# Performance work log

Measured on AMD Instinct MI355X. Metric: run time of the kernel, lower is better.

## Reference

```python
import jax, jax.numpy as jnp
import numpy as np


def setup_inputs() -> dict:
    key = jax.random.key(0)
    ks = jax.random.split(key, 6)
    B, IN, H, OUT = 4096, 1024, 2048, 256
    s1 = 1.0 / np.sqrt(IN)
    s2 = 1.0 / np.sqrt(H)
    return {
        "x": jax.random.normal(ks[0], (B, IN), dtype=jnp.float32),
        "W1": jax.random.uniform(ks[1], (H, IN), jnp.float32, -s1, s1),
        "b1": jax.random.uniform(ks[2], (H,), jnp.float32, -s1, s1),
        "W2": jax.random.uniform(ks[3], (OUT, H), jnp.float32, -s2, s2),
        "b2": jax.random.uniform(ks[4], (OUT,), jnp.float32, -s2, s2),
        "tau_mem": jnp.float32(10.0),
        "tau_syn": jnp.float32(5.0),
        "v_thresh": jnp.float32(1.0),
        "v_reset": jnp.float32(0.0),
        "v_mem0": jnp.zeros((B, H), jnp.float32),
        "i_syn0": jnp.zeros((B, H), jnp.float32),
        "time_steps": 32,
    }


def reference(x, W1, b1, W2, b2, tau_mem, tau_syn, v_thresh, v_reset, v_mem0, i_syn0, time_steps):
    dt = jnp.float32(1.0)
    # fc1(x)/time_steps is identical every step in the original loop; compute once.
    cur = (x @ W1.T + b1) / jnp.float32(time_steps)  # [B, H]

    def step(carry, _):
        v, i = carry
        i = i - (dt / tau_syn) * i + cur
        v = v - (dt / tau_mem) * v + i
        s = (v >= v_thresh).astype(x.dtype)
        v = v * (1.0 - s) + v_reset * s
        return (v, i), s

    (_, _), spikes = jax.lax.scan(step, (v_mem0, i_syn0), None, length=time_steps)
    total_spikes = spikes.sum(axis=0)  # [B, H]
    output = total_spikes @ W2.T + b2  # [B, OUT]
    return output, total_spikes
```

## Files before the change

kernel.cpp:

```cpp
#include <hip/hip_runtime.h>
#include <hip/hip_bf16.h>
#include <stdint.h>

typedef __attribute__((ext_vector_type(8))) short bf16x8;
typedef __attribute__((ext_vector_type(4))) float f32x4;

__device__ __forceinline__ float vmulf(float a, float b) {
    float d; asm volatile("v_mul_f32 %0, %1, %2" : "=v"(d) : "v"(a), "v"(b)); return d;
}
__device__ __forceinline__ float vaddf(float a, float b) {
    float d; asm volatile("v_add_f32 %0, %1, %2" : "=v"(d) : "v"(a), "v"(b)); return d;
}
__device__ __forceinline__ float vsubf(float a, float b) {
    float d; asm volatile("v_sub_f32 %0, %1, %2" : "=v"(d) : "v"(a), "v"(b)); return d;
}

__device__ __forceinline__ short bf16h(float v) {
    __hip_bfloat16 h = __float2bfloat16(v);
    return *(short*)&h;
}
__device__ __forceinline__ float bf16f(short s) {
    return __uint_as_float(((unsigned int)(unsigned short)s) << 16);
}
__device__ __forceinline__ void split2(float v, short& h, short& m) {
    h = bf16h(v);
    m = bf16h(__fsub_rn(v, bf16f(h)));
}

__device__ __forceinline__ float decode_scalar(const void* p, float dflt) {
    float f = *(const float*)p;
    if (!(f == f) || fabsf(f) > 1.0e6f) return dflt;
    return f;
}
__device__ __forceinline__ int decode_ts(const void* p) {
    int w = *(const int*)p;
    if (w >= 1 && w <= 100000) return w;
    return 32;
}

__device__ __forceinline__ void gl16(const float* g, float* l) {
    __builtin_amdgcn_global_load_lds(
        (const __attribute__((address_space(1))) unsigned int*)g,
        (__attribute__((address_space(3))) unsigned int*)l, 16, 0, 0);
}

#define LDA 36

__global__ __launch_bounds__(256) void k1_panel_gemm(
    const float* __restrict__ X,
    const float* __restrict__ W1,
    float* __restrict__ P0,
    float* __restrict__ P1,
    int M, int N, int K, int KC)
{
    __shared__ __align__(16) float As[2][128][16];
    __shared__ __align__(16) float Bs[2][128][16];

    const int t  = threadIdx.x;
    const int tx = t & 15;
    const int ty = t >> 4;
    const int m0 = blockIdx.x * 128;
    const int n0 = blockIdx.y * 128;
    const int kz = blockIdx.z * KC;
    float* __restrict__ Pout = blockIdx.z ? P1 : P0;

    float p[8][8] = {};

    const int w     = t >> 6;
    const int l     = t & 63;
    const int r0    = 32 * w + (l >> 2);
    const int r1    = r0 + 16;
    const int selem = ((l & 3) ^ ((l >> 3) & 3)) << 2;
    const int oa0 = (m0 + r0) * K + selem;
    const int oa1 = (m0 + r1) * K + selem;
    const int ob0 = (n0 + r0) * K + selem;
    const int ob1 = (n0 + r1) * K + selem;

    gl16(X  + oa0 + kz, &As[0][32 * w][0]);
    gl16(X  + oa1 + kz, &As[0][32 * w + 16][0]);
    gl16(W1 + ob0 + kz, &Bs[0][32 * w][0]);
    gl16(W1 + ob1 + kz, &Bs[0][32 * w + 16][0]);

    const int cax = (ty >> 1) & 3;
    const int cbx = (tx >> 1) & 3;

    const int nch = KC >> 4;
    for (int c = 0; c < nch; ++c) {
        __syncthreads();
        const int d = c & 1;
        if (c + 1 < nch) {
            const int kn = kz + ((c + 1) << 4);
            const int dn = d ^ 1;
            gl16(X  + oa0 + kn, &As[dn][32 * w][0]);
            gl16(X  + oa1 + kn, &As[dn][32 * w + 16][0]);
            gl16(W1 + ob0 + kn, &Bs[dn][32 * w][0]);
            gl16(W1 + ob1 + kn, &Bs[dn][32 * w + 16][0]);
        }
        #pragma unroll
        for (int g = 0; g < 4; ++g) {
            float4 bfv[8];
            const int cb = (g ^ cbx) << 2;
            #pragma unroll
            for (int j = 0; j < 8; ++j)
                bfv[j] = *(const float4*)&Bs[d][tx + 16 * j][cb];
            const int ca = (g ^ cax) << 2;
            #pragma unroll
            for (int i = 0; i < 8; ++i) {
                const float4 af = *(const float4*)&As[d][ty + 16 * i][ca];
                #pragma unroll
                for (int kk = 0; kk < 4; ++kk) {
                    const float a = ((const float*)&af)[kk];
                    #pragma unroll
                    for (int j = 0; j < 8; ++j)
                        p[i][j] = __builtin_fmaf(a, ((const float*)&bfv[j])[kk], p[i][j]);
                }
            }
        }
    }

    #pragma unroll
    for (int i = 0; i < 8; ++i) {
        const size_t rowb = (size_t)(m0 + ty + 16 * i) * N;
        #pragma unroll
        for (int j = 0; j < 8; ++j)
            Pout[rowb + n0 + tx + 16 * j] = p[i][j];
    }
}

__global__ __launch_bounds__(256) void k1_combine_scan(
    const float* __restrict__ P0,
    const float* __restrict__ P1,
    const float* __restrict__ b1,
    const void* tau_mem_p, const void* tau_syn_p,
    const void* v_thresh_p, const void* v_reset_p, const void* ts_p,
    float* __restrict__ spikes, int N, int total4)
{
    const int idx4 = blockIdx.x * 256 + threadIdx.x;
    if (idx4 >= total4) return;

    const float tau_m = decode_scalar(tau_mem_p, 10.0f);
    const float tau_s = decode_scalar(tau_syn_p, 5.0f);
    const float vth   = decode_scalar(v_thresh_p, 1.0f);
    const float vrs   = decode_scalar(v_reset_p, 0.0f);
    const int   ts    = decode_ts(ts_p);
    const float rs    = 1.0f / tau_s;
    const float rm    = 1.0f / tau_m;
    const float ivts  = 1.0f / (float)ts;

    const float4 a = ((const float4*)P0)[idx4];
    const float4 b = ((const float4*)P1)[idx4];
    const int col0 = (idx4 * 4) % N;
    const float4 bb = *(const float4*)&b1[col0];

    float cur[4], iv[4], vv[4], cnt[4];
    const float av[4] = {a.x, a.y, a.z, a.w};
    const float bv[4] = {b.x, b.y, b.z, b.w};
    const float bbv[4] = {bb.x, bb.y, bb.z, bb.w};
    #pragma unroll
    for (int e = 0; e < 4; ++e) {
        const float c = vaddf(av[e], bv[e]);
        cur[e] = vmulf(vaddf(c, bbv[e]), ivts);
        iv[e] = 0.0f; vv[e] = 0.0f; cnt[e] = 0.0f;
    }
    for (int tt = 0; tt < ts; ++tt) {
        #pragma unroll
        for (int e = 0; e < 4; ++e) {
            iv[e] = vaddf(vsubf(iv[e], vmulf(rs, iv[e])), cur[e]);
            vv[e] = vaddf(vsubf(vv[e], vmulf(rm, vv[e])), iv[e]);
            const bool s = (vv[e] >= vth);
            cnt[e] += s ? 1.0f : 0.0f;
            vv[e]   = s ? vrs : vv[e];
        }
    }
    ((float4*)spikes)[idx4] = make_float4(cnt[0], cnt[1], cnt[2], cnt[3]);
}

__global__ __launch_bounds__(256) void k1_f32chain_snn(
    const float* __restrict__ X, const float* __restrict__ W1,
    const float* __restrict__ b1,
    const void* tau_mem_p, const void* tau_syn_p,
    const void* v_thresh_p, const void* v_reset_p, const void* ts_p,
    float* __restrict__ spikes, int M, int N, int K, int f0)
{
    __shared__ float As[128][LDA];
    __shared__ float Bs[128][LDA];

    const int t  = threadIdx.x;
    const int tx = t & 15;
    const int ty = t >> 4;
    const int m0 = blockIdx.x * 128;
    const int n0 = blockIdx.y * 128;

    float c[8][8] = {};
    float p[8][8] = {};

    for (int k0 = 0; k0 < K; k0 += 32) {
        #pragma unroll
        for (int cc = 0; cc < 4; ++cc) {
            const int li  = cc * 256 + t;
            const int row = li >> 3;
            const int q   = li & 7;
            *(float4*)&As[row][q * 4] =
                *(const float4*)&X[(size_t)(m0 + row) * K + k0 + q * 4];
            *(float4*)&Bs[row][q * 4] =
                *(const float4*)&W1[(size_t)(n0 + row) * K + k0 + q * 4];
        }
        __syncthreads();
        #pragma unroll
        for (int g = 0; g < 8; ++g) {
            float4 af[8], bf[8];
            #pragma unroll
            for (int i = 0; i < 8; ++i)
                af[i] = *(const float4*)&As[ty + 16 * i][g * 4];
            #pragma unroll
            for (int j = 0; j < 8; ++j)
                bf[j] = *(const float4*)&Bs[tx + 16 * j][g * 4];
            #pragma unroll
            for (int kk = 0; kk < 4; ++kk) {
                #pragma unroll
                for (int i = 0; i < 8; ++i) {
                    const float a = ((const float*)&af[i])[kk];
                    #pragma unroll
                    for (int j = 0; j < 8; ++j)
                        p[i][j] = __builtin_fmaf(a, ((const float*)&bf[j])[kk], p[i][j]);
                }
            }
        }
        __syncthreads();
        const int ke = k0 + 32;
        if (ke == f0 || ke == K) {
            #pragma unroll
            for (int i = 0; i < 8; ++i)
                #pragma unroll
                for (int j = 0; j < 8; ++j) {
                    c[i][j] = vaddf(c[i][j], p[i][j]);
                    p[i][j] = 0.0f;
                }
        }
    }

    const float tau_m = decode_scalar(tau_mem_p, 10.0f);
    const float tau_s = decode_scalar(tau_syn_p, 5.0f);
    const float vth   = decode_scalar(v_thresh_p, 1.0f);
    const float vrs   = decode_scalar(v_reset_p, 0.0f);
    const int   ts    = decode_ts(ts_p);
    const float rs    = 1.0f / tau_s;
    const float rm    = 1.0f / tau_m;
    const float ivts  = 1.0f / (float)ts;

    #pragma unroll
    for (int j = 0; j < 8; ++j) {
        const int col    = n0 + tx + 16 * j;
        const float bias = b1[col];
        float cur[8], iv[8], vv[8], cnt[8];
        #pragma unroll
        for (int i = 0; i < 8; ++i) {
            cur[i] = vmulf(vaddf(c[i][j], bias), ivts);
            iv[i] = 0.0f; vv[i] = 0.0f; cnt[i] = 0.0f;
        }
        for (int tt = 0; tt < ts; ++tt) {
            #pragma unroll
            for (int i = 0; i < 8; ++i) {
                iv[i] = vaddf(vsubf(iv[i], vmulf(rs, iv[i])), cur[i]);
                vv[i] = vaddf(vsubf(vv[i], vmulf(rm, vv[i])), iv[i]);
                const bool s = (vv[i] >= vth);
                cnt[i] += s ? 1.0f : 0.0f;
                vv[i]   = s ? vrs : vv[i];
            }
        }
        #pragma unroll
        for (int i = 0; i < 8; ++i)
            spikes[(size_t)(m0 + ty + 16 * i) * N + col] = cnt[i];
    }
}

__global__ __launch_bounds__(256) void k2_partial(
    const float* __restrict__ S, const float* __restrict__ W2,
    float* __restrict__ Pt,
    int M, int N2, int K2, int KC2)
{
    __shared__ __align__(16) short Sa[64 * 32];
    __shared__ __align__(16) short Bh[64 * 32];
    __shared__ __align__(16) short Bm[64 * 32];

    const int t    = threadIdx.x;
    const int l    = t & 63;
    const int w    = t >> 6;
    const int quad = l >> 4;
    const int r    = l & 15;
    const int wm   = w & 1;
    const int wn   = w >> 1;

    const int m0 = blockIdx.x * 64;
    const int n0 = blockIdx.y * 64;
    const int kz = blockIdx.z * KC2;
    float* __restrict__ outp = Pt + (size_t)blockIdx.z * M * N2;

    f32x4 acc[2][2] = {};

    for (int k0 = kz; k0 < kz + KC2; k0 += 32) {
        #pragma unroll
        for (int cc = 0; cc < 2; ++cc) {
            const int li  = cc * 256 + t;
            const int row = li >> 3;
            const int q   = li & 7;
            const float4 vs = *(const float4*)&S[(size_t)(m0 + row) * K2 + k0 + q * 4];
            *(short4*)&Sa[row * 32 + q * 4] =
                make_short4(bf16h(vs.x), bf16h(vs.y), bf16h(vs.z), bf16h(vs.w));
            const float4 vb = *(const float4*)&W2[(size_t)(n0 + row) * K2 + k0 + q * 4];
            short h[4], m_[4];
            split2(vb.x, h[0], m_[0]); split2(vb.y, h[1], m_[1]);
            split2(vb.z, h[2], m_[2]); split2(vb.w, h[3], m_[3]);
            *(short4*)&Bh[row * 32 + q * 4] = make_short4(h[0], h[1], h[2], h[3]);
            *(short4*)&Bm[row * 32 + q * 4] = make_short4(m_[0], m_[1], m_[2], m_[3]);
        }
        __syncthreads();

        bf16x8 af[2], bh[2], bm[2];
        #pragma unroll
        for (int i = 0; i < 2; ++i) {
            af[i] = *(const bf16x8*)&Sa[(wm * 32 + i * 16 + r) * 32 + quad * 8];
            bh[i] = *(const bf16x8*)&Bh[(wn * 32 + i * 16 + r) * 32 + quad * 8];
            bm[i] = *(const bf16x8*)&Bm[(wn * 32 + i * 16 + r) * 32 + quad * 8];
        }
        #pragma unroll
        for (int i = 0; i < 2; ++i)
            #pragma unroll
            for (int j = 0; j < 2; ++j) {
                acc[i][j] = __builtin_amdgcn_mfma_f32_16x16x32_bf16(af[i], bh[j], acc[i][j], 0, 0, 0);
                acc[i][j] = __builtin_amdgcn_mfma_f32_16x16x32_bf16(af[i], bm[j], acc[i][j], 0, 0, 0);
            }
        __syncthreads();
    }

    #pragma unroll
    for (int j = 0; j < 2; ++j) {
        const int col = n0 + wn * 32 + j * 16 + r;
        #pragma unroll
        for (int i = 0; i < 2; ++i) {
            const int rowb = m0 + wm * 32 + i * 16 + quad * 4;
            #pragma unroll
            for (int e = 0; e < 4; ++e)
                outp[(size_t)(rowb + e) * N2 + col] = acc[i][j][e];
        }
    }
}

__global__ __launch_bounds__(256) void k2_combine(
    const float* __restrict__ Pt, const float* __restrict__ b2,
    float* __restrict__ out, int N2, int total4, size_t stride4)
{
    const int idx4 = blockIdx.x * 256 + threadIdx.x;
    if (idx4 >= total4) return;
    float4 s = ((const float4*)Pt)[idx4];
    #pragma unroll
    for (int z = 1; z < 4; ++z) {
        const float4 v = ((const float4*)Pt)[stride4 * z + idx4];
        s.x += v.x; s.y += v.y; s.z += v.z; s.w += v.w;
    }
    const float4 bb = *(const float4*)&b2[(idx4 * 4) % N2];
    s.x += bb.x; s.y += bb.y; s.z += bb.z; s.w += bb.w;
    ((float4*)out)[idx4] = s;
}

__global__ __launch_bounds__(256) void k2_gemm(
    const float* __restrict__ S, const float* __restrict__ W2,
    const float* __restrict__ b2, float* __restrict__ out,
    int M, int N2, int K2)
{
    __shared__ __align__(16) short Sa[64 * 32];
    __shared__ __align__(16) short Bh[64 * 32];
    __shared__ __align__(16) short Bm[64 * 32];

    const int t    = threadIdx.x;
    const int l    = t & 63;
    const int w    = t >> 6;
    const int quad = l >> 4;
    const int r    = l & 15;
    const int wm   = w & 1;
    const int wn   = w >> 1;

    const int m0 = blockIdx.x * 64;
    const int n0 = blockIdx.y * 64;

    f32x4 acc[2][2] = {};

    for (int k0 = 0; k0 < K2; k0 += 32) {
        #pragma unroll
        for (int cc = 0; cc < 2; ++cc) {
            const int li  = cc * 256 + t;
            const int row = li >> 3;
            const int q   = li & 7;
            const float4 vs = *(const float4*)&S[(size_t)(m0 + row) * K2 + k0 + q * 4];
            *(short4*)&Sa[row * 32 + q * 4] =
                make_short4(bf16h(vs.x), bf16h(vs.y), bf16h(vs.z), bf16h(vs.w));
            const float4 vb = *(const float4*)&W2[(size_t)(n0 + row) * K2 + k0 + q * 4];
            short h[4], m_[4];
            split2(vb.x, h[0], m_[0]); split2(vb.y, h[1], m_[1]);
            split2(vb.z, h[2], m_[2]); split2(vb.w, h[3], m_[3]);
            *(short4*)&Bh[row * 32 + q * 4] = make_short4(h[0], h[1], h[2], h[3]);
            *(short4*)&Bm[row * 32 + q * 4] = make_short4(m_[0], m_[1], m_[2], m_[3]);
        }
        __syncthreads();

        bf16x8 af[2], bh[2], bm[2];
        #pragma unroll
        for (int i = 0; i < 2; ++i) {
            af[i] = *(const bf16x8*)&Sa[(wm * 32 + i * 16 + r) * 32 + quad * 8];
            bh[i] = *(const bf16x8*)&Bh[(wn * 32 + i * 16 + r) * 32 + quad * 8];
            bm[i] = *(const bf16x8*)&Bm[(wn * 32 + i * 16 + r) * 32 + quad * 8];
        }
        #pragma unroll
        for (int i = 0; i < 2; ++i)
            #pragma unroll
            for (int j = 0; j < 2; ++j) {
                acc[i][j] = __builtin_amdgcn_mfma_f32_16x16x32_bf16(af[i], bh[j], acc[i][j], 0, 0, 0);
                acc[i][j] = __builtin_amdgcn_mfma_f32_16x16x32_bf16(af[i], bm[j], acc[i][j], 0, 0, 0);
            }
        __syncthreads();
    }

    #pragma unroll
    for (int j = 0; j < 2; ++j) {
        const int col = n0 + wn * 32 + j * 16 + r;
        const float bias = b2[col];
        #pragma unroll
        for (int i = 0; i < 2; ++i) {
            const int rowb = m0 + wm * 32 + i * 16 + quad * 4;
            #pragma unroll
            for (int e = 0; e < 4; ++e)
                out[(size_t)(rowb + e) * N2 + col] = __fadd_rn(acc[i][j][e], bias);
        }
    }
}

extern "C" void kernel_launch(void* const* d_in, const int* in_sizes, int n_in,
                              void* d_out, int out_size, void* d_ws, size_t ws_size,
                              hipStream_t stream) {
    (void)n_in; (void)out_size;

    const float* X  = (const float*)d_in[0];
    const float* W1 = (const float*)d_in[1];
    const float* b1 = (const float*)d_in[2];
    const float* W2 = (const float*)d_in[3];
    const float* b2 = (const float*)d_in[4];
    const void* tau_mem = d_in[5];
    const void* tau_syn = d_in[6];
    const void* vth     = d_in[7];
    const void* vrs     = d_in[8];
    const void* ts      = d_in[11];

    const int H   = in_sizes[2];
    const int IN  = in_sizes[1] / H;
    const int OUT = in_sizes[4];
    const int B   = in_sizes[0] / IN;

    float* out    = (float*)d_out;
    float* spikes = out + (size_t)B * OUT;

    const int KC = 512;
    const size_t panel_bytes = (size_t)B * H * sizeof(float);
    const bool ws_ok = (IN == 2 * KC) && (ws_size >= panel_bytes) &&
                       ((uintptr_t)d_ws % 16 == 0);

    if (ws_ok) {
        float* P1 = (float*)d_ws;
        dim3 g1(B / 128, H / 128, 2);
        k1_panel_gemm<<<g1, 256, 0, stream>>>(X, W1, spikes, P1, B, H, IN, KC);

        const int total4 = (B * H) / 4;
        k1_combine_scan<<<(total4 + 255) / 256, 256, 0, stream>>>(
            spikes, P1, b1, tau_mem, tau_syn, vth, vrs, ts, spikes, H, total4);
    } else {
        dim3 g1(B / 128, H / 128);
        k1_f32chain_snn<<<g1, 256, 0, stream>>>(X, W1, b1, tau_mem, tau_syn, vth, vrs, ts,
                                                spikes, B, H, IN, KC);
    }

    const int KC2 = 512;
    const size_t k2_part_bytes = 4 * (size_t)B * OUT * sizeof(float);
    if (ws_ok && H == 4 * KC2 && ws_size >= k2_part_bytes) {
        float* Pt = (float*)d_ws;
        dim3 g2(B / 64, OUT / 64, 4);
        k2_partial<<<g2, 256, 0, stream>>>(spikes, W2, Pt, B, OUT, H, KC2);
        const int total4 = (B * OUT) / 4;
        k2_combine<<<(total4 + 255) / 256, 256, 0, stream>>>(
            Pt, b2, out, OUT, total4, (size_t)B * OUT / 4);
    } else {
        dim3 g2(B / 64, OUT / 64);
        k2_gemm<<<g2, 256, 0, stream>>>(spikes, W2, b2, out, B, OUT, H);
    }
}
```

Measured before the change: 416.3 us.

## Fuse layer-1 GEMM with LIF scan, dropping split-K panels and workspace round trip

Replaces the split-K panel GEMM plus separate combine/scan kernel with one kernel that computes a 64x128 tile over the full K, merges the two 512-wide K halves in registers, and runs the 32-step LIF recurrence in-register before writing spike counts. This removes writing and rereading two B x H float panels through global memory and one kernel launch. In exchange the grid loses the split-K z dimension, gets twice as many blocks along M with a smaller M tile, and the serial scan now runs inside the GEMM kernel rather than in a separate fully parallel pass.

After: 464.5 us. 1.12x slower.

```diff
diff --git a/kernel.cpp b/kernel.cpp
--- a/kernel.cpp
+++ b/kernel.cpp
@@ -46,53 +46,53 @@
 
 #define LDA 36
 
-__global__ __launch_bounds__(256) void k1_panel_gemm(
+__global__ __launch_bounds__(256) void k1_fused_snn(
     const float* __restrict__ X,
     const float* __restrict__ W1,
-    float* __restrict__ P0,
-    float* __restrict__ P1,
-    int M, int N, int K, int KC)
+    const float* __restrict__ b1,
+    const void* tau_mem_p, const void* tau_syn_p,
+    const void* v_thresh_p, const void* v_reset_p, const void* ts_p,
+    float* __restrict__ spikes, int M, int N, int K)
 {
-    __shared__ __align__(16) float As[2][128][16];
+    __shared__ __align__(16) float As[2][64][16];
     __shared__ __align__(16) float Bs[2][128][16];
 
     const int t  = threadIdx.x;
     const int tx = t & 15;
     const int ty = t >> 4;
-    const int m0 = blockIdx.x * 128;
+    const int m0 = blockIdx.x * 64;
     const int n0 = blockIdx.y * 128;
-    const int kz = blockIdx.z * KC;
-    float* __restrict__ Pout = blockIdx.z ? P1 : P0;
-
-    float p[8][8] = {};
+
+    float p[4][8] = {};
+    float c[4][8];
 
     const int w     = t >> 6;
     const int l     = t & 63;
-    const int r0    = 32 * w + (l >> 2);
-    const int r1    = r0 + 16;
+    const int rr    = l >> 2;
     const int selem = ((l & 3) ^ ((l >> 3) & 3)) << 2;
-    const int oa0 = (m0 + r0) * K + selem;
-    const int oa1 = (m0 + r1) * K + selem;
-    const int ob0 = (n0 + r0) * K + selem;
-    const int ob1 = (n0 + r1) * K + selem;
-
-    gl16(X  + oa0 + kz, &As[0][32 * w][0]);
-    gl16(X  + oa1 + kz, &As[0][32 * w + 16][0]);
-    gl16(W1 + ob0 + kz, &Bs[0][32 * w][0]);
-    gl16(W1 + ob1 + kz, &Bs[0][32 * w + 16][0]);
+    const int ra  = 16 * w + rr;
+    const int rb0 = 32 * w + rr;
+    const int rb1 = rb0 + 16;
+    const int oa  = (m0 + ra ) * K + selem;
+    const int ob0 = (n0 + rb0) * K + selem;
+    const int ob1 = (n0 + rb1) * K + selem;
+
+    gl16(X  + oa , &As[0][16 * w][0]);
+    gl16(W1 + ob0, &Bs[0][32 * w][0]);
+    gl16(W1 + ob1, &Bs[0][32 * w + 16][0]);
 
     const int cax = (ty >> 1) & 3;
     const int cbx = (tx >> 1) & 3;
 
-    const int nch = KC >> 4;
-    for (int c = 0; c < nch; ++c) {
-        __syncthreads();
-        const int d = c & 1;
-        if (c + 1 < nch) {
-            const int kn = kz + ((c + 1) << 4);
+    const int nch = K >> 4;
+    int nf = 0;
+    for (int ch = 0; ch < nch; ++ch) {
+        __syncthreads();
+        const int d = ch & 1;
+        if (ch + 1 < nch) {
+            const int kn = (ch + 1) << 4;
             const int dn = d ^ 1;
-            gl16(X  + oa0 + kn, &As[dn][32 * w][0]);
-            gl16(X  + oa1 + kn, &As[dn][32 * w + 16][0]);
+            gl16(X  + oa  + kn, &As[dn][16 * w][0]);
             gl16(W1 + ob0 + kn, &Bs[dn][32 * w][0]);
             gl16(W1 + ob1 + kn, &Bs[dn][32 * w + 16][0]);
         }
@@ -105,7 +105,7 @@
                 bfv[j] = *(const float4*)&Bs[d][tx + 16 * j][cb];
             const int ca = (g ^ cax) << 2;
             #pragma unroll
-            for (int i = 0; i < 8; ++i) {
+            for (int i = 0; i < 4; ++i) {
                 const float4 af = *(const float4*)&As[d][ty + 16 * i][ca];
                 #pragma unroll
                 for (int kk = 0; kk < 4; ++kk) {
@@ -116,27 +116,22 @@
                 }
             }
         }
-    }
-
-    #pragma unroll
-    for (int i = 0; i < 8; ++i) {
-        const size_t rowb = (size_t)(m0 + ty + 16 * i) * N;
-        #pragma unroll
-        for (int j = 0; j < 8; ++j)
-            Pout[rowb + n0 + tx + 16 * j] = p[i][j];
-    }
-}
-
-__global__ __launch_bounds__(256) void k1_combine_scan(
-    const float* __restrict__ P0,
-    const float* __restrict__ P1,
-    const float* __restrict__ b1,
-    const void* tau_mem_p, const void* tau_syn_p,
-    const void* v_thresh_p, const void* v_reset_p, const void* ts_p,
-    float* __restrict__ spikes, int N, int total4)
-{
-    const int idx4 = blockIdx.x * 256 + threadIdx.x;
-    if (idx4 >= total4) return;
+        const int ke = (ch + 1) << 4;
+        if ((ke & 511) == 0 || ke == K) {
+            if (nf == 0) {
+                #pragma unroll
+                for (int i = 0; i < 4; ++i)
+                    #pragma unroll
+                    for (int j = 0; j < 8; ++j) { c[i][j] = p[i][j]; p[i][j] = 0.0f; }
+            } else {
+                #pragma unroll
+                for (int i = 0; i < 4; ++i)
+                    #pragma unroll
+                    for (int j = 0; j < 8; ++j) { c[i][j] = vaddf(c[i][j], p[i][j]); p[i][j] = 0.0f; }
+            }
+            ++nf;
+        }
+    }
 
     const float tau_m = decode_scalar(tau_mem_p, 10.0f);
     const float tau_s = decode_scalar(tau_syn_p, 5.0f);
@@ -147,32 +142,30 @@
     const float rm    = 1.0f / tau_m;
     const float ivts  = 1.0f / (float)ts;
 
-    const float4 a = ((const float4*)P0)[idx4];
-    const float4 b = ((const float4*)P1)[idx4];
-    const int col0 = (idx4 * 4) % N;
-    const float4 bb = *(const float4*)&b1[col0];
-
-    float cur[4], iv[4], vv[4], cnt[4];
-    const float av[4] = {a.x, a.y, a.z, a.w};
-    const float bv[4] = {b.x, b.y, b.z, b.w};
-    const float bbv[4] = {bb.x, bb.y, bb.z, bb.w};
     #pragma unroll
-    for (int e = 0; e < 4; ++e) {
-        const float c = vaddf(av[e], bv[e]);
-        cur[e] = vmulf(vaddf(c, bbv[e]), ivts);
-        iv[e] = 0.0f; vv[e] = 0.0f; cnt[e] = 0.0f;
-    }
-    for (int tt = 0; tt < ts; ++tt) {
-        #pragma unroll
-        for (int e = 0; e < 4; ++e) {
-            iv[e] = vaddf(vsubf(iv[e], vmulf(rs, iv[e])), cur[e]);
-            vv[e] = vaddf(vsubf(vv[e], vmulf(rm, vv[e])), iv[e]);
-            const bool s = (vv[e] >= vth);
-            cnt[e] += s ? 1.0f : 0.0f;
-            vv[e]   = s ? vrs : vv[e];
-        }
-    }
-    ((float4*)spikes)[idx4] = make_float4(cnt[0], cnt[1], cnt[2], cnt[3]);
+    for (int j = 0; j < 8; ++j) {
+        const int col    = n0 + tx + 16 * j;
+        const float bias = b1[col];
+        float cur[4], iv[4], vv[4], cnt[4];
+        #pragma unroll
+        for (int i = 0; i < 4; ++i) {
+            cur[i] = vmulf(vaddf(c[i][j], bias), ivts);
+            iv[i] = 0.0f; vv[i] = 0.0f; cnt[i] = 0.0f;
+        }
+        for (int tt = 0; tt < ts; ++tt) {
+            #pragma unroll
+            for (int i = 0; i < 4; ++i) {
+                iv[i] = vaddf(vsubf(iv[i], vmulf(rs, iv[i])), cur[i]);
+                vv[i] = vaddf(vsubf(vv[i], vmulf(rm, vv[i])), iv[i]);
+                const bool s = (vv[i] >= vth);
+                cnt[i] += s ? 1.0f : 0.0f;
+                vv[i]   = s ? vrs : vv[i];
+            }
+        }
+        #pragma unroll
+        for (int i = 0; i < 4; ++i)
+            spikes[(size_t)(m0 + ty + 16 * i) * N + col] = cnt[i];
+    }
 }
 
 __global__ __launch_bounds__(256) void k1_f32chain_snn(
@@ -458,28 +451,22 @@
     float* out    = (float*)d_out;
     float* spikes = out + (size_t)B * OUT;
 
-    const int KC = 512;
-    const size_t panel_bytes = (size_t)B * H * sizeof(float);
-    const bool ws_ok = (IN == 2 * KC) && (ws_size >= panel_bytes) &&
-                       ((uintptr_t)d_ws % 16 == 0);
-
-    if (ws_ok) {
-        float* P1 = (float*)d_ws;
-        dim3 g1(B / 128, H / 128, 2);
-        k1_panel_gemm<<<g1, 256, 0, stream>>>(X, W1, spikes, P1, B, H, IN, KC);
-
-        const int total4 = (B * H) / 4;
-        k1_combine_scan<<<(total4 + 255) / 256, 256, 0, stream>>>(
-            spikes, P1, b1, tau_mem, tau_syn, vth, vrs, ts, spikes, H, total4);
+    if ((IN % 32) == 0 && (B % 64) == 0 && (H % 128) == 0) {
+        dim3 g1(B / 64, H / 128);
+        k1_fused_snn<<<g1, 256, 0, stream>>>(X, W1, b1, tau_mem, tau_syn, vth, vrs, ts,
+                                             spikes, B, H, IN);
     } else {
         dim3 g1(B / 128, H / 128);
         k1_f32chain_snn<<<g1, 256, 0, stream>>>(X, W1, b1, tau_mem, tau_syn, vth, vrs, ts,
-                                                spikes, B, H, IN, KC);
+                                                spikes, B, H, IN, 512);
     }
 
     const int KC2 = 512;
     const size_t k2_part_bytes = 4 * (size_t)B * OUT * sizeof(float);
-    if (ws_ok && H == 4 * KC2 && ws_size >= k2_part_bytes) {
+    const bool ws_ok2 = (H == 4 * KC2) && (ws_size >= k2_part_bytes) &&
+                        ((uintptr_t)d_ws % 16 == 0) &&
+                        (B % 64 == 0) && (OUT % 64 == 0);
+    if (ws_ok2) {
         float* Pt = (float*)d_ws;
         dim3 g2(B / 64, OUT / 64, 4);
         k2_partial<<<g2, 256, 0, stream>>>(spikes, W2, Pt, B, OUT, H, KC2);
```
